# Performance work log

Hardware: AMD Instinct MI355X
Metric: run time of the kernel (lower is better)

Reference implementation:

```python
import jax, jax.numpy as jnp
import numpy as np

DIM = 3072
HEADS = 24
HEAD_DIM = 128
MLP_HIDDEN = int(DIM * 3.0)   # 9216
EPS = 1e-6
B, S = 1, 4096


def setup_inputs() -> dict:
    key = jax.random.key(0)
    ks = jax.random.split(key, 9)
    fused_out = 3 * DIM + 2 * MLP_HIDDEN  # 27648
    std_in = 1.0 / np.sqrt(DIM)
    return {
        "hidden_states": jax.random.normal(ks[0], (B, S, DIM), jnp.float32),
        "temb_mod": jax.random.normal(ks[1], (B, 3 * DIM), jnp.float32),
        "rotary_cos": jax.random.uniform(ks[2], (S, HEAD_DIM), jnp.float32),
        "rotary_sin": jax.random.uniform(ks[3], (S, HEAD_DIM), jnp.float32),
        "w_qkv_mlp": jax.random.normal(ks[4], (DIM, fused_out), jnp.float32) * std_in,
        "w_out_attn": jax.random.normal(ks[5], (DIM, DIM), jnp.float32) * std_in,
        "w_out_mlp": jax.random.normal(ks[6], (MLP_HIDDEN, DIM), jnp.float32) * (1.0 / np.sqrt(MLP_HIDDEN)),
        "norm_q_w": jnp.ones((HEAD_DIM,), jnp.float32),
        "norm_k_w": jnp.ones((HEAD_DIM,), jnp.float32),
    }


def _rms_norm(x, w):
    var = jnp.mean(jnp.square(x), axis=-1, keepdims=True)
    return x * jax.lax.rsqrt(var + EPS) * w


def _apply_rope(x, cos, sin):
    # x: [B,H,S,D]; cos/sin: [S,D]. Interleaved (diffusers FLUX) rotation.
    xr = x.reshape(*x.shape[:-1], HEAD_DIM // 2, 2)
    x_re, x_im = xr[..., 0], xr[..., 1]
    x_rot = jnp.stack([-x_im, x_re], axis=-1).reshape(x.shape)
    return x * cos + x_rot * sin


def reference(hidden_states, temb_mod, rotary_cos, rotary_sin,
              w_qkv_mlp, w_out_attn, w_out_mlp, norm_q_w, norm_k_w):
    residual = hidden_states
    # modulation split: shift, scale, gate each [B,1,D]
    shift, scale, gate = jnp.split(temb_mod[:, None, :], 3, axis=-1)
    # LayerNorm (no affine)
    mu = jnp.mean(hidden_states, axis=-1, keepdims=True)
    var = jnp.mean(jnp.square(hidden_states - mu), axis=-1, keepdims=True)
    ln = (hidden_states - mu) * jax.lax.rsqrt(var + EPS)
    h = ln * (1.0 + scale) + shift
    # fused QKV + MLP projection
    qkv_mlp = jnp.einsum('bsd,df->bsf', h, w_qkv_mlp)
    qkv, mlp_gate_up = jnp.split(qkv_mlp, [3 * DIM], axis=-1)
    q, k, v = jnp.split(qkv, 3, axis=-1)
    to_heads = lambda t: t.reshape(B, S, HEADS, HEAD_DIM).transpose(0, 2, 1, 3)
    q, k, v = to_heads(q), to_heads(k), to_heads(v)
    q = _apply_rope(_rms_norm(q, norm_q_w), rotary_cos, rotary_sin)
    k = _apply_rope(_rms_norm(k, norm_k_w), rotary_cos, rotary_sin)
    # attention
    scores = jnp.einsum('bhqd,bhkd->bhqk', q, k) / np.sqrt(HEAD_DIM).astype(np.float32)
    attn = jnp.einsum('bhqk,bhkd->bhqd', jax.nn.softmax(scores, axis=-1), v)
    attn = attn.transpose(0, 2, 1, 3).reshape(B, S, DIM)
    # SwiGLU
    a, b = jnp.split(mlp_gate_up, 2, axis=-1)
    mlp_out = jax.nn.silu(a) * b
    out = jnp.einsum('bsd,de->bse', attn, w_out_attn) + jnp.einsum('bsm,md->bsd', mlp_out, w_out_mlp)
    return residual + gate * out
```

## Files before the change

### kernel.cpp

```cpp
#include <hip/hip_runtime.h>
#include <stdint.h>
#include <math.h>

#define DIM 3072
#define SEQ 4096
#define NH 24
#define HD 128
#define MLP 9216
#define FUSED 27648
#define SD FUSED
#define K2 12288

typedef __attribute__((ext_vector_type(8))) short short8;
typedef __attribute__((ext_vector_type(4))) float f32x4;

__device__ __forceinline__ float bf2f(uint16_t b){ uint32_t x = ((uint32_t)b)<<16; return __builtin_bit_cast(float,x); }
__device__ __forceinline__ uint16_t f2bf(float f){
  uint32_t x = __builtin_bit_cast(uint32_t,f);
  x += 0x7fffu + ((x>>16)&1u);
  return (uint16_t)(x>>16);
}
__device__ __forceinline__ void gl_lds16(const void* g, void* l){
  __builtin_amdgcn_global_load_lds((const __attribute__((address_space(1))) void*)g,
                                   (__attribute__((address_space(3))) void*)l, 16, 0, 0);
}

__global__ __launch_bounds__(256) void castT_kernel(const float* __restrict__ src,
                                                    uint16_t* __restrict__ dst,
                                                    int K, int N, int dstStride){
  __shared__ float tile[32][33];
  int t = threadIdx.x;
  int n0 = blockIdx.x<<5, k0 = blockIdx.y<<5;
  int r = t>>3, c4 = (t&7)<<2;
  float4 v = *(const float4*)&src[(size_t)(k0+r)*N + n0 + c4];
  tile[r][c4] = v.x; tile[r][c4+1] = v.y; tile[r][c4+2] = v.z; tile[r][c4+3] = v.w;
  __syncthreads();
  int n = t>>3, kc = (t&7)<<2;
  ushort4 o;
  o.x = f2bf(tile[kc  ][n]);
  o.y = f2bf(tile[kc+1][n]);
  o.z = f2bf(tile[kc+2][n]);
  o.w = f2bf(tile[kc+3][n]);
  *(ushort4*)&dst[(size_t)(n0+n)*dstStride + k0 + kc] = o;
}

__global__ __launch_bounds__(256) void ln_mod_kernel(const float* __restrict__ x,
                                                     const float* __restrict__ temb,
                                                     uint16_t* __restrict__ h){
  int s = blockIdx.x;
  int t = threadIdx.x;
  const float4* row = (const float4*)(x + (size_t)s*DIM);
  float4 v[3];
  float sum=0.f, ss=0.f;
  #pragma unroll
  for (int i=0;i<3;i++){
    v[i] = row[t + i*256];
    sum += v[i].x+v[i].y+v[i].z+v[i].w;
    ss  += v[i].x*v[i].x + v[i].y*v[i].y + v[i].z*v[i].z + v[i].w*v[i].w;
  }
  #pragma unroll
  for (int off=32; off; off>>=1){ sum += __shfl_xor(sum, off, 64); ss += __shfl_xor(ss, off, 64); }
  __shared__ float red[8];
  int lane = t&63, w = t>>6;
  if (lane==0){ red[w]=sum; red[w+4]=ss; }
  __syncthreads();
  sum = red[0]+red[1]+red[2]+red[3];
  ss  = red[4]+red[5]+red[6]+red[7];
  float mu = sum*(1.f/DIM);
  float var = ss*(1.f/DIM) - mu*mu;
  float rs = rsqrtf(var + 1e-6f);
  uint16_t* hrow = h + (size_t)s*DIM;
  #pragma unroll
  for (int i=0;i<3;i++){
    int c = (t + i*256)*4;
    float4 sc = *(const float4*)&temb[DIM + c];
    float4 sh = *(const float4*)&temb[c];
    ushort4 o;
    o.x = f2bf((v[i].x - mu)*rs*(1.f+sc.x) + sh.x);
    o.y = f2bf((v[i].y - mu)*rs*(1.f+sc.y) + sh.y);
    o.z = f2bf((v[i].z - mu)*rs*(1.f+sc.z) + sh.z);
    o.w = f2bf((v[i].w - mu)*rs*(1.f+sc.w) + sh.w);
    *(ushort4*)&hrow[c] = o;
  }
}

#define STAGE_HT(SRC, LDSB, KOFF) do{ \
    gl_lds16((SRC) + (KOFF), (LDSB) + (size_t)t*8); \
    gl_lds16((SRC) + r64K + (KOFF), (LDSB) + (size_t)(t+512)*8); \
  }while(0)

#define PH_READ4(d0,d1,d2,d3, BASE, MIA, MIB) \
    d0 = *(const short8*)&(BASE)[(MIA)*1024 + pk0]; \
    d1 = *(const short8*)&(BASE)[(MIA)*1024 + pk1]; \
    d2 = *(const short8*)&(BASE)[(MIB)*1024 + pk0]; \
    d3 = *(const short8*)&(BASE)[(MIB)*1024 + pk1];

#define PH_MFMA4(s0,s1,s2,s3, MI0, MI1) \
    _Pragma("unroll") \
    for (int ni=0; ni<4; ni++){ \
      acc[MI0][ni] = __builtin_amdgcn_mfma_f32_16x16x32_bf16(s0, bfr[ni][0], acc[MI0][ni], 0,0,0); \
      acc[MI1][ni] = __builtin_amdgcn_mfma_f32_16x16x32_bf16(s2, bfr[ni][0], acc[MI1][ni], 0,0,0); \
      acc[MI0][ni] = __builtin_amdgcn_mfma_f32_16x16x32_bf16(s1, bfr[ni][1], acc[MI0][ni], 0,0,0); \
      acc[MI1][ni] = __builtin_amdgcn_mfma_f32_16x16x32_bf16(s3, bfr[ni][1], acc[MI1][ni], 0,0,0); \
    }

#define PH_COMMIT \
    __builtin_amdgcn_sched_barrier(0); \
    __builtin_amdgcn_s_barrier(); \
    __builtin_amdgcn_s_setprio(1);

#define PH_CLOSE \
    __builtin_amdgcn_s_setprio(0); \
    __builtin_amdgcn_sched_barrier(0); \
    __builtin_amdgcn_s_barrier();

template<bool OUT_BF16, bool FINAL>
__global__ __launch_bounds__(512,2) void gemm256_kernel(const uint16_t* __restrict__ A,
                                                        const uint16_t* __restrict__ BT,
                                                        void* __restrict__ Cout,
                                                        const float* __restrict__ resid,
                                                        const float* __restrict__ temb,
                                                        int M, int N, int K){
  __shared__ alignas(16) uint16_t As[2][2][128*64];
  __shared__ alignas(16) uint16_t Bs[2][2][128*64];
  const int t = threadIdx.x, lane = t&63, w = t>>6;
  const int G = gridDim.x, cpx = G>>3;
  const int b = blockIdx.x;
  const int b2 = (b&7)*cpx + (b>>3);
  const int mt = M>>8;
  const int n_t = b2/mt, m_t = b2 - n_t*mt;
  const size_t m0 = (size_t)m_t<<8, n0 = (size_t)n_t<<8;
  const int wm = (w>>2)<<7, wn = (w&3)<<6;
  const int lr = lane&15, q4 = lane>>4;
  const int r0 = t>>3;
  const int g0 = (t&7) ^ (r0&7);
  const uint16_t* Asrc = A  + (m0 + r0)*(size_t)K + g0*8;
  const uint16_t* Bsrc = BT + (n0 + r0)*(size_t)K + g0*8;
  const size_t r64K = (size_t)64*K, r128K = (size_t)128*K;
  const int halfA = w>>2, halfB = (w&3)>>1, rbB = wn&64;
  const uint16_t* ArdE = &As[0][halfA][0] + lr*64;
  const uint16_t* BrdE = &Bs[0][halfB][0] + (rbB+lr)*64;
  const uint16_t* ArdO = ArdE + 16384;
  const uint16_t* BrdO = BrdE + 16384;
  const int x7 = lr&7;
  const int pk0 = (q4^x7)<<3, pk1 = ((q4|4)^x7)<<3;
  STAGE_HT(Bsrc, &Bs[0][0][0], (size_t)0);
  STAGE_HT(Bsrc, &Bs[0][1][0], r128K);
  STAGE_HT(Asrc, &As[0][0][0], (size_t)0);
  STAGE_HT(Asrc, &As[0][1][0], r128K);
  STAGE_HT(Bsrc, &Bs[1][0][0], (size_t)64);
  STAGE_HT(Bsrc, &Bs[1][1][0], r128K + 64);
  asm volatile("s_waitcnt vmcnt(4)" ::: "memory");
  __builtin_amdgcn_s_barrier();
  short8 pa0,pa1,pa2,pa3, qa0,qa1,qa2,qa3;
  short8 bfr[4][2];
  PH_READ4(pa0,pa1,pa2,pa3, ArdE, 0, 1);
  #pragma unroll
  for (int ni=0; ni<4; ni++){
    bfr[ni][0] = *(const short8*)&BrdE[ni*1024 + pk0];
    bfr[ni][1] = *(const short8*)&BrdE[ni*1024 + pk1];
  }
  f32x4 acc[8][4] = {};
  const int NT = K>>6;
  for (int T=0; T<NT; ++T){
    const uint16_t* AbC = (T&1) ? ArdO : ArdE;
    const uint16_t* AbN = (T&1) ? ArdE : ArdO;
    const uint16_t* BbN = (T&1) ? BrdE : BrdO;
    uint16_t* AsN0 = &As[(T&1)^1][0][0];
    uint16_t* AsN1 = &As[(T&1)^1][1][0];
    uint16_t* BsC0 = &Bs[T&1][0][0];
    uint16_t* BsC1 = &Bs[T&1][1][0];
    const bool stA = (T+1<NT), stB = (T+2<NT);
    const size_t kA = (size_t)(T+1)<<6, kB = (size_t)(T+2)<<6;
    PH_READ4(qa0,qa1,qa2,qa3, AbC, 2, 3);
    if (stA){ STAGE_HT(Asrc, AsN0, kA); }
    PH_COMMIT
    PH_MFMA4(pa0,pa1,pa2,pa3, 0, 1)
    PH_CLOSE
    PH_READ4(pa0,pa1,pa2,pa3, AbC, 4, 5);
    if (stA){ STAGE_HT(Asrc, AsN1, kA + r128K); }
    PH_COMMIT
    PH_MFMA4(qa0,qa1,qa2,qa3, 2, 3)
    PH_CLOSE
    PH_READ4(qa0,qa1,qa2,qa3, AbC, 6, 7);
    if (stB){ STAGE_HT(Bsrc, BsC0, kB); }
    PH_COMMIT
    PH_MFMA4(pa0,pa1,pa2,pa3, 4, 5)
    PH_CLOSE
    if (stB){ STAGE_HT(Bsrc, BsC1, kB + r128K); }
    PH_COMMIT
    PH_MFMA4(qa0,qa1,qa2,qa3, 6, 7)
    __builtin_amdgcn_s_setprio(0);
    if (T+1 < NT){
      if (stB){ asm volatile("s_waitcnt vmcnt(4)" ::: "memory"); }
      else    { asm volatile("s_waitcnt vmcnt(0)" ::: "memory"); }
      PH_READ4(pa0,pa1,pa2,pa3, AbN, 0, 1);
      #pragma unroll
      for (int ni=0; ni<4; ni++){
        bfr[ni][0] = *(const short8*)&BbN[ni*1024 + pk0];
        bfr[ni][1] = *(const short8*)&BbN[ni*1024 + pk1];
      }
    }
    __builtin_amdgcn_sched_barrier(0);
    __builtin_amdgcn_s_barrier();
  }
  #pragma unroll
  for (int mi=0; mi<8; mi++){
    #pragma unroll
    for (int ni=0; ni<4; ni++){
      const size_t col = n0 + wn + ni*16 + lr;
      const float gate = FINAL ? temb[2*DIM + col] : 0.f;
      #pragma unroll
      for (int r=0; r<4; r++){
        const size_t row = m0 + wm + mi*16 + (q4<<2) + r;
        const size_t idx = row*(size_t)N + col;
        float vv = acc[mi][ni][r];
        if (FINAL) vv = resid[idx] + gate*vv;
        if (OUT_BF16) ((uint16_t*)Cout)[idx] = f2bf(vv);
        else          ((float*)Cout)[idx] = vv;
      }
    }
  }
}

__global__ __launch_bounds__(256) void qk_rope_kernel(uint16_t* __restrict__ qkv,
                                                      const float* __restrict__ cosb,
                                                      const float* __restrict__ sinb,
                                                      const float* __restrict__ wq,
                                                      const float* __restrict__ wk){
  int t = threadIdx.x, lane = t&63, w = t>>6;
  int pair = blockIdx.x*4 + w;
  int s = pair/24, hh = pair - s*24;
  int d0 = lane*2;
  float c0 = cosb[s*HD + d0], c1 = cosb[s*HD + d0+1];
  float sn0 = sinb[s*HD + d0], sn1 = sinb[s*HD + d0+1];
  #pragma unroll
  for (int which=0; which<2; ++which){
    uint16_t* p = qkv + (size_t)s*SD + which*DIM + hh*HD + d0;
    const float* ww = which ? wk : wq;
    uint32_t u = *(const uint32_t*)p;
    float x0 = bf2f((uint16_t)(u&0xffffu)), x1 = bf2f((uint16_t)(u>>16));
    float ssum = x0*x0 + x1*x1;
    #pragma unroll
    for (int off=32; off; off>>=1) ssum += __shfl_xor(ssum, off, 64);
    float r = rsqrtf(ssum*(1.f/HD) + 1e-6f);
    float xn0 = x0*r*ww[d0], xn1 = x1*r*ww[d0+1];
    float y0 = xn0*c0 - xn1*sn0;
    float y1 = xn1*c1 + xn0*sn1;
    *(uint32_t*)p = (uint32_t)f2bf(y0) | ((uint32_t)f2bf(y1)<<16);
  }
}

__global__ __launch_bounds__(256) void attn_kernel(const uint16_t* __restrict__ qkv,
                                                   uint16_t* __restrict__ out){
  __shared__ alignas(16) uint16_t QP[64*128];
  __shared__ alignas(16) uint16_t Ks[64*128];
  __shared__ alignas(16) uint16_t Vt[128*64];
  int t = threadIdx.x, lane = t&63, w = t>>6;
  int q0 = blockIdx.x<<6, h = blockIdx.y;
  int lr = lane&15, q4 = lane>>4, lk = q4<<3;
  const uint16_t* qb = qkv + (size_t)q0*SD + h*HD;
  #pragma unroll
  for (int i=0;i<4;i++){
    int c = t + i*256;
    gl_lds16((const char*)(qb + (size_t)(c>>4)*SD) + ((c&15)<<4), (char*)QP + c*16);
  }
  __syncthreads();
  short8 qf[4];
  #pragma unroll
  for (int kc=0;kc<4;kc++) qf[kc] = *(const short8*)&QP[(w*16+lr)*128 + kc*32 + lk];
  __syncthreads();
  float m_i[4] = {-3.0e38f,-3.0e38f,-3.0e38f,-3.0e38f};
  float l_i[4] = {0.f,0.f,0.f,0.f};
  f32x4 o[8] = {};
  const uint16_t* kb = qkv + (size_t)DIM + h*HD;
  const uint16_t* vb = qkv + (size_t)(2*DIM) + h*HD;
  uint16_t* Pw = QP + w*(16*64);
  const float scale = 0.08838834764831845f;
  for (int kt=0; kt<64; ++kt){
    const uint16_t* kbt = kb + (size_t)(kt<<6)*SD;
    const uint16_t* vbt = vb + (size_t)(kt<<6)*SD;
    __syncthreads();
    #pragma unroll
    for (int i=0;i<4;i++){
      int c = t + i*256;
      int row = c>>4, gd = c&15;
      uint4 vv = *(const uint4*)(kbt + (size_t)row*SD + gd*8);
      *(uint4*)&Ks[row*128 + ((gd ^ (row&15))<<3)] = vv;
    }
    #pragma unroll
    for (int i=0;i<8;i++){
      int idx = t + i*256;
      int rp = idx>>6;
      int k0 = rp<<1, d0 = lane<<1;
      uint32_t u0 = *(const uint32_t*)(vbt + (size_t)k0*SD + d0);
      uint32_t u1 = *(const uint32_t*)(vbt + (size_t)(k0+1)*SD + d0);
      int pos = (((rp>>2) ^ (lane&7))<<3) + (k0&7);
      *(uint32_t*)&Vt[(d0<<6) + pos]     = (u0&0xffffu) | (u1<<16);
      *(uint32_t*)&Vt[((d0+1)<<6) + pos] = (u0>>16) | (u1&0xffff0000u);
    }
    __syncthreads();
    f32x4 sa[4];
    #pragma unroll
    for (int nk=0;nk<4;nk++){
      sa[nk] = (f32x4){0.f,0.f,0.f,0.f};
      #pragma unroll
      for (int kc=0;kc<4;kc++){
        short8 kf = *(const short8*)&Ks[(nk*16+lr)*128 + (((kc*4+q4) ^ lr)<<3)];
        sa[nk] = __builtin_amdgcn_mfma_f32_16x16x32_bf16(qf[kc], kf, sa[nk], 0,0,0);
      }
      sa[nk] *= scale;
    }
    float alpha[4], psum[4];
    #pragma unroll
    for (int r=0;r<4;r++){
      float mx = fmaxf(fmaxf(sa[0][r], sa[1][r]), fmaxf(sa[2][r], sa[3][r]));
      mx = fmaxf(mx, __shfl_xor(mx, 1, 64));
      mx = fmaxf(mx, __shfl_xor(mx, 2, 64));
      mx = fmaxf(mx, __shfl_xor(mx, 4, 64));
      mx = fmaxf(mx, __shfl_xor(mx, 8, 64));
      float mn = fmaxf(m_i[r], mx);
      alpha[r] = __expf(m_i[r] - mn);
      m_i[r] = mn;
      psum[r] = 0.f;
    }
    int prow = q4<<2;
    #pragma unroll
    for (int nk=0;nk<4;nk++){
      #pragma unroll
      for (int r=0;r<4;r++){
        float p = __expf(sa[nk][r] - m_i[r]);
        psum[r] += p;
        int key = nk*16 + lr;
        Pw[(prow+r)*64 + ((((key>>3) ^ (prow+r))&7)<<3) + (key&7)] = f2bf(p);
      }
    }
    #pragma unroll
    for (int r=0;r<4;r++){
      float ps = psum[r];
      ps += __shfl_xor(ps, 1, 64);
      ps += __shfl_xor(ps, 2, 64);
      ps += __shfl_xor(ps, 4, 64);
      ps += __shfl_xor(ps, 8, 64);
      l_i[r] = l_i[r]*alpha[r] + ps;
    }
    #pragma unroll
    for (int nd=0;nd<8;nd++){
      f32x4 t4 = o[nd];
      t4[0]*=alpha[0]; t4[1]*=alpha[1]; t4[2]*=alpha[2]; t4[3]*=alpha[3];
      o[nd]=t4;
    }
    #pragma unroll
    for (int kc=0;kc<2;kc++){
      short8 pf = *(const short8*)&Pw[lr*64 + ((((kc*4+q4) ^ lr)&7)<<3)];
      #pragma unroll
      for (int nd=0;nd<8;nd++){
        int d = nd*16 + lr;
        short8 vf = *(const short8*)&Vt[(d<<6) + ((((kc*4+q4) ^ ((lr>>1)&7)))<<3)];
        o[nd] = __builtin_amdgcn_mfma_f32_16x16x32_bf16(pf, vf, o[nd], 0,0,0);
      }
    }
  }
  uint16_t* ob = out + (size_t)(q0 + w*16)*K2 + h*HD;
  #pragma unroll
  for (int r=0;r<4;r++){
    float inv = 1.f/l_i[r];
    #pragma unroll
    for (int nd=0;nd<8;nd++)
      ob[(size_t)(q4*4 + r)*K2 + nd*16 + lr] = f2bf(o[nd][r]*inv);
  }
}

__global__ __launch_bounds__(256) void swiglu_kernel(const uint16_t* __restrict__ qkv,
                                                     uint16_t* __restrict__ mlp){
  size_t idx = ((size_t)blockIdx.x*256 + threadIdx.x)*4;
  size_t s = idx/MLP, j = idx - s*MLP;
  const uint16_t* pa = qkv + s*SD + 3*DIM + j;
  const uint16_t* pb = pa + MLP;
  ushort4 ua = *(const ushort4*)pa, ub = *(const ushort4*)pb;
  ushort4 o;
  float a, b;
  a = bf2f(ua.x); b = bf2f(ub.x); o.x = f2bf(a*b/(1.f+__expf(-a)));
  a = bf2f(ua.y); b = bf2f(ub.y); o.y = f2bf(a*b/(1.f+__expf(-a)));
  a = bf2f(ua.z); b = bf2f(ub.z); o.z = f2bf(a*b/(1.f+__expf(-a)));
  a = bf2f(ua.w); b = bf2f(ub.w); o.w = f2bf(a*b/(1.f+__expf(-a)));
  *(ushort4*)(mlp + s*K2 + j) = o;
}

extern "C" void kernel_launch(void* const* d_in, const int* in_sizes, int n_in,
                              void* d_out, int out_size, void* d_ws, size_t ws_size,
                              hipStream_t stream){
  (void)in_sizes; (void)n_in; (void)out_size;
  const float* hs   = (const float*)d_in[0];
  const float* temb = (const float*)d_in[1];
  const float* rcos = (const float*)d_in[2];
  const float* rsin = (const float*)d_in[3];
  const float* w1   = (const float*)d_in[4];
  const float* wa   = (const float*)d_in[5];
  const float* wm   = (const float*)d_in[6];
  const float* nqw  = (const float*)d_in[7];
  const float* nkw  = (const float*)d_in[8];

  char* ws = (char*)d_ws;
  const size_t off_w1T  = 0;
  const size_t off_woT  = 169869312ULL;
  const size_t off_h    = 245366784ULL;
  const size_t off_qkv  = 270532608ULL;
  const size_t off_ap   = 497025024ULL;
  const size_t needed   = 597688320ULL;
  if (ws_size < needed) return;

  uint16_t* w1T  = (uint16_t*)(ws + off_w1T);
  uint16_t* woT  = (uint16_t*)(ws + off_woT);
  uint16_t* hbuf = (uint16_t*)(ws + off_h);
  uint16_t* qkv  = (uint16_t*)(ws + off_qkv);
  uint16_t* ap   = (uint16_t*)(ws + off_ap);

  castT_kernel<<<dim3(FUSED/32, DIM/32), 256, 0, stream>>>(w1, w1T, DIM, FUSED, DIM);
  castT_kernel<<<dim3(DIM/32,  DIM/32),  256, 0, stream>>>(wa, woT, DIM, DIM, K2);
  castT_kernel<<<dim3(DIM/32,  MLP/32),  256, 0, stream>>>(wm, woT + DIM, MLP, DIM, K2);
  ln_mod_kernel<<<SEQ, 256, 0, stream>>>(hs, temb, hbuf);
  gemm256_kernel<true,false><<<(SEQ/256)*(FUSED/256), 512, 0, stream>>>(hbuf, w1T, qkv, nullptr, nullptr, SEQ, FUSED, DIM);
  qk_rope_kernel<<<SEQ*NH/4, 256, 0, stream>>>(qkv, rcos, rsin, nqw, nkw);
  attn_kernel<<<dim3(SEQ/64, NH), 256, 0, stream>>>(qkv, ap);
  swiglu_kernel<<<(SEQ*(size_t)MLP/4)/256, 256, 0, stream>>>(qkv, ap + DIM);
  gemm256_kernel<false,true><<<(SEQ/256)*(DIM/256), 512, 0, stream>>>(ap, woT, d_out, hs, temb, SEQ, DIM, K2);
}
```

Measured before the change: 2.447 ms.

## Simplify GEMM main loop to single-barrier double buffering

Replaces the staggered 8-wave ping-pong schedule, which had per-phase barriers and B prefetched two tiles ahead, with a plain double-buffered loop. Each iteration issues all four A/B stage loads for the next K tile, interleaves LDS fragment reads with the MFMA groups, then waits on everything and takes one barrier. This removes three intra-iteration barriers but loses the deeper B prefetch and the waits scheduled early around each phase, so global load latency may be hidden less well.

```diff
diff --git a/kernel.cpp b/kernel.cpp
--- a/kernel.cpp
+++ b/kernel.cpp
@@ -96,23 +96,15 @@
     d3 = *(const short8*)&(BASE)[(MIB)*1024 + pk1];
 
 #define PH_MFMA4(s0,s1,s2,s3, MI0, MI1) \
+    __builtin_amdgcn_s_setprio(1); \
     _Pragma("unroll") \
     for (int ni=0; ni<4; ni++){ \
       acc[MI0][ni] = __builtin_amdgcn_mfma_f32_16x16x32_bf16(s0, bfr[ni][0], acc[MI0][ni], 0,0,0); \
       acc[MI1][ni] = __builtin_amdgcn_mfma_f32_16x16x32_bf16(s2, bfr[ni][0], acc[MI1][ni], 0,0,0); \
       acc[MI0][ni] = __builtin_amdgcn_mfma_f32_16x16x32_bf16(s1, bfr[ni][1], acc[MI0][ni], 0,0,0); \
       acc[MI1][ni] = __builtin_amdgcn_mfma_f32_16x16x32_bf16(s3, bfr[ni][1], acc[MI1][ni], 0,0,0); \
-    }
-
-#define PH_COMMIT \
-    __builtin_amdgcn_sched_barrier(0); \
-    __builtin_amdgcn_s_barrier(); \
-    __builtin_amdgcn_s_setprio(1);
-
-#define PH_CLOSE \
-    __builtin_amdgcn_s_setprio(0); \
-    __builtin_amdgcn_sched_barrier(0); \
-    __builtin_amdgcn_s_barrier();
+    } \
+    __builtin_amdgcn_s_setprio(0);
 
 template<bool OUT_BF16, bool FINAL>
 __global__ __launch_bounds__(512,2) void gemm256_kernel(const uint16_t* __restrict__ A,
@@ -143,66 +135,46 @@
   const uint16_t* ArdO = ArdE + 16384;
   const uint16_t* BrdO = BrdE + 16384;
   const int x7 = lr&7;
-  const int pk0 = (q4^x7)<<3, pk1 = ((q4|4)^x7)<<3;
+  const int pk0 = (q4^x7)<<3, pk1 = ((q4|4)<<3)^(x7<<3);
   STAGE_HT(Bsrc, &Bs[0][0][0], (size_t)0);
   STAGE_HT(Bsrc, &Bs[0][1][0], r128K);
   STAGE_HT(Asrc, &As[0][0][0], (size_t)0);
   STAGE_HT(Asrc, &As[0][1][0], r128K);
-  STAGE_HT(Bsrc, &Bs[1][0][0], (size_t)64);
-  STAGE_HT(Bsrc, &Bs[1][1][0], r128K + 64);
-  asm volatile("s_waitcnt vmcnt(4)" ::: "memory");
+  asm volatile("s_waitcnt vmcnt(0)" ::: "memory");
   __builtin_amdgcn_s_barrier();
-  short8 pa0,pa1,pa2,pa3, qa0,qa1,qa2,qa3;
-  short8 bfr[4][2];
-  PH_READ4(pa0,pa1,pa2,pa3, ArdE, 0, 1);
-  #pragma unroll
-  for (int ni=0; ni<4; ni++){
-    bfr[ni][0] = *(const short8*)&BrdE[ni*1024 + pk0];
-    bfr[ni][1] = *(const short8*)&BrdE[ni*1024 + pk1];
-  }
+  __builtin_amdgcn_sched_barrier(0);
   f32x4 acc[8][4] = {};
   const int NT = K>>6;
   for (int T=0; T<NT; ++T){
-    const uint16_t* AbC = (T&1) ? ArdO : ArdE;
-    const uint16_t* AbN = (T&1) ? ArdE : ArdO;
-    const uint16_t* BbN = (T&1) ? BrdE : BrdO;
-    uint16_t* AsN0 = &As[(T&1)^1][0][0];
-    uint16_t* AsN1 = &As[(T&1)^1][1][0];
-    uint16_t* BsC0 = &Bs[T&1][0][0];
-    uint16_t* BsC1 = &Bs[T&1][1][0];
-    const bool stA = (T+1<NT), stB = (T+2<NT);
-    const size_t kA = (size_t)(T+1)<<6, kB = (size_t)(T+2)<<6;
-    PH_READ4(qa0,qa1,qa2,qa3, AbC, 2, 3);
-    if (stA){ STAGE_HT(Asrc, AsN0, kA); }
-    PH_COMMIT
+    const uint16_t* Ab = (T&1) ? ArdO : ArdE;
+    const uint16_t* Bb = (T&1) ? BrdO : BrdE;
+    const int nx = (T&1)^1;
+    const bool st = (T+1<NT);
+    const size_t kN = (size_t)(T+1)<<6;
+    short8 bfr[4][2];
+    #pragma unroll
+    for (int ni=0; ni<4; ni++){
+      bfr[ni][0] = *(const short8*)&Bb[ni*1024 + pk0];
+      bfr[ni][1] = *(const short8*)&Bb[ni*1024 + pk1];
+    }
+    short8 pa0,pa1,pa2,pa3, qa0,qa1,qa2,qa3;
+    PH_READ4(pa0,pa1,pa2,pa3, Ab, 0, 1);
+    if (st){
+      STAGE_HT(Asrc, &As[nx][0][0], kN);
+      STAGE_HT(Asrc, &As[nx][1][0], kN + r128K);
+      STAGE_HT(Bsrc, &Bs[nx][0][0], kN);
+      STAGE_HT(Bsrc, &Bs[nx][1][0], kN + r128K);
+    }
+    PH_READ4(qa0,qa1,qa2,qa3, Ab, 2, 3);
     PH_MFMA4(pa0,pa1,pa2,pa3, 0, 1)
-    PH_CLOSE
-    PH_READ4(pa0,pa1,pa2,pa3, AbC, 4, 5);
-    if (stA){ STAGE_HT(Asrc, AsN1, kA + r128K); }
-    PH_COMMIT
+    PH_READ4(pa0,pa1,pa2,pa3, Ab, 4, 5);
     PH_MFMA4(qa0,qa1,qa2,qa3, 2, 3)
-    PH_CLOSE
-    PH_READ4(qa0,qa1,qa2,qa3, AbC, 6, 7);
-    if (stB){ STAGE_HT(Bsrc, BsC0, kB); }
-    PH_COMMIT
+    PH_READ4(qa0,qa1,qa2,qa3, Ab, 6, 7);
     PH_MFMA4(pa0,pa1,pa2,pa3, 4, 5)
-    PH_CLOSE
-    if (stB){ STAGE_HT(Bsrc, BsC1, kB + r128K); }
-    PH_COMMIT
     PH_MFMA4(qa0,qa1,qa2,qa3, 6, 7)
-    __builtin_amdgcn_s_setprio(0);
-    if (T+1 < NT){
-      if (stB){ asm volatile("s_waitcnt vmcnt(4)" ::: "memory"); }
-      else    { asm volatile("s_waitcnt vmcnt(0)" ::: "memory"); }
-      PH_READ4(pa0,pa1,pa2,pa3, AbN, 0, 1);
-      #pragma unroll
-      for (int ni=0; ni<4; ni++){
-        bfr[ni][0] = *(const short8*)&BbN[ni*1024 + pk0];
-        bfr[ni][1] = *(const short8*)&BbN[ni*1024 + pk1];
-      }
-    }
+    asm volatile("s_waitcnt vmcnt(0) lgkmcnt(0)" ::: "memory");
+    __builtin_amdgcn_s_barrier();
     __builtin_amdgcn_sched_barrier(0);
-    __builtin_amdgcn_s_barrier();
   }
   #pragma unroll
   for (int mi=0; mi<8; mi++){
```

Result: no change. 2.426 ms (-0.9%).
